# Kernel optimization log

Hardware: AMD Instinct MI355X
Metric: run time of the kernel (lower is better)

## Reference

```python
import jax, jax.numpy as jnp
import numpy as np

B, T, Tc = 64, 256, 16
VW, VC, L = 100000, 128, 25
CE, CH = 25, 25          # char embed / char lstm hidden per direction
WE, WH = 100, 100        # word embed / word lstm hidden per direction (bi -> 200)
DW = WE + 2 * CH         # 150, word-LSTM input dim


def lstm(x, Wih, Whh, b):
    """Unidirectional LSTM over time axis 1. x: [N, S, D] -> [N, S, H]. PyTorch gate order i,f,g,o."""
    N = x.shape[0]
    H = Whh.shape[0]
    x_t = jnp.swapaxes(x, 0, 1)  # [S, N, D]

    def step(carry, xt):
        h, c = carry
        g = xt @ Wih + h @ Whh + b
        i, f, gg, o = jnp.split(g, 4, axis=-1)
        c = jax.nn.sigmoid(f) * c + jax.nn.sigmoid(i) * jnp.tanh(gg)
        h = jax.nn.sigmoid(o) * jnp.tanh(c)
        return (h, c), h

    h0 = jnp.zeros((N, H), x.dtype)
    _, hs = jax.lax.scan(step, (h0, h0), x_t)
    return jnp.swapaxes(hs, 0, 1)  # [N, S, H]


def crf_nll(em, tags, trans, start, end):
    """Negative log-likelihood of linear-chain CRF (no mask; full-length sequences)."""
    # gold path score
    em_score = jnp.take_along_axis(em, tags[:, :, None], axis=2).squeeze(-1).sum(axis=1)
    tr_score = trans[tags[:, :-1], tags[:, 1:]].sum(axis=1)
    gold = start[tags[:, 0]] + em_score + tr_score + end[tags[:, -1]]
    # forward algorithm (log partition)
    alpha0 = start[None, :] + em[:, 0]  # [B, L]

    def step(alpha, e_t):
        # alpha: [B, L] prev-tag scores; trans: [L, L]; e_t: [B, L]
        new = jax.nn.logsumexp(alpha[:, :, None] + trans[None, :, :] + e_t[:, None, :], axis=1)
        return new, None

    alpha, _ = jax.lax.scan(step, alpha0, jnp.swapaxes(em[:, 1:], 0, 1))
    logZ = jax.nn.logsumexp(alpha + end[None, :], axis=1)
    return jnp.sum(logZ - gold)


def setup_inputs():
    key = jax.random.key(0)
    ks = jax.random.split(key, 24)
    f = lambda i, shape: jax.random.normal(ks[i], shape, jnp.float32) * 0.1
    return {
        "tok_tensor": jax.random.randint(ks[0], (B, T), 0, VW),
        "tag_tensor": jax.random.randint(ks[1], (B, T), 0, L),
        "lengths": jnp.full((B,), T, jnp.int32),
        "char_tensor": jax.random.randint(ks[2], (B * T, Tc), 0, VC),
        "char_lengths": jax.random.randint(ks[3], (B * T,), 1, Tc + 1),
        "char_tensor_recover": jax.random.permutation(ks[4], B * T),
        "word_emb": f(5, (VW, WE)),
        "char_emb": f(6, (VC, CE)),
        "cWih_f": f(7, (CE, 4 * CH)), "cWhh_f": f(8, (CH, 4 * CH)), "cb_f": jnp.zeros((4 * CH,), jnp.float32),
        "cWih_b": f(9, (CE, 4 * CH)), "cWhh_b": f(10, (CH, 4 * CH)), "cb_b": jnp.zeros((4 * CH,), jnp.float32),
        "wWih_f": f(11, (DW, 4 * WH)), "wWhh_f": f(12, (WH, 4 * WH)), "wb_f": jnp.zeros((4 * WH,), jnp.float32),
        "wWih_b": f(13, (DW, 4 * WH)), "wWhh_b": f(14, (WH, 4 * WH)), "wb_b": jnp.zeros((4 * WH,), jnp.float32),
        "W_tag": f(15, (2 * WH, L)), "b_tag": jnp.zeros((L,), jnp.float32),
        "trans": f(16, (L, L)), "start": f(17, (L,)), "end": f(18, (L,)),
    }


def reference(tok_tensor, tag_tensor, lengths, char_tensor, char_lengths, char_tensor_recover,
              word_emb, char_emb,
              cWih_f, cWhh_f, cb_f, cWih_b, cWhh_b, cb_b,
              wWih_f, wWhh_f, wb_f, wWih_b, wWhh_b, wb_b,
              W_tag, b_tag, trans, start, end):
    N = char_tensor.shape[0]  # B*T words
    # ---- char BiLSTM: last hidden of each direction per word ----
    ce = char_emb[char_tensor]                      # [N, Tc, CE]
    last = char_lengths - 1
    hf = lstm(ce, cWih_f, cWhh_f, cb_f)             # [N, Tc, CH]
    h_fwd = hf[jnp.arange(N), last]                 # forward last valid hidden
    # backward: reverse each word within its length, scan, take hidden at step len-1
    t_ar = jnp.arange(Tc)[None, :]
    rev_idx = jnp.where(t_ar < char_lengths[:, None], char_lengths[:, None] - 1 - t_ar, t_ar)
    ce_rev = jnp.take_along_axis(ce, rev_idx[:, :, None], axis=1)
    hb = lstm(ce_rev, cWih_b, cWhh_b, cb_b)
    h_bwd = hb[jnp.arange(N), last]
    char_feat = jnp.concatenate([h_fwd, h_bwd], axis=-1)[char_tensor_recover].reshape(B, T, 2 * CH)
    # ---- concat word + char features (dropout = identity in eval) ----
    x = jnp.concatenate([word_emb[tok_tensor], char_feat], axis=-1)  # [B, T, DW]
    # ---- word BiLSTM (full-length sequences) ----
    h_f = lstm(x, wWih_f, wWhh_f, wb_f)
    h_b = jnp.flip(lstm(jnp.flip(x, axis=1), wWih_b, wWhh_b, wb_b), axis=1)
    seq = jnp.concatenate([h_f, h_b], axis=-1)       # [B, T, 2*WH]
    # ---- emissions + CRF NLL ----
    em = seq @ W_tag + b_tag                         # [B, T, L]
    return crf_nll(em, tag_tensor, trans, start, end)
```

## Files before the change

kernel.cpp:

```cpp
#include <hip/hip_runtime.h>
#include <hip/hip_bf16.h>

#define NB 64
#define NT 256
#define TC 16
#define NL 25
#define NWORDS 16384
#define DWd 150
#define WEd 100
#define WPB 5

__device__ __forceinline__ float sigf(float x){ return __fdividef(1.f, 1.f + __expf(-x)); }
__device__ __forceinline__ float tanhf_(float x){
    float ax = fabsf(x);
    float e = __expf(-2.f*ax);
    float r = (1.f - e) * __fdividef(1.f, 1.f + e);
    return copysignf(r, x);
}
__device__ __forceinline__ float RL(float v, int k){
    return __int_as_float(__builtin_amdgcn_readlane(__float_as_int(v), k));
}

__global__ void k_zero(int* __restrict__ meta){
  if (threadIdx.x < 34) meta[threadIdx.x] = 0;
}
__global__ __launch_bounds__(256) void k_hist(const int* __restrict__ char_lengths,
                                              int* __restrict__ hist){
  __shared__ int lh[16];
  int tid = threadIdx.x;
  if (tid < 16) lh[tid] = 0;
  __syncthreads();
  int w = blockIdx.x*256 + tid;
  atomicAdd(&lh[char_lengths[w]-1], 1);
  __syncthreads();
  if (tid < 16) atomicAdd(&hist[tid], lh[tid]);
}
__global__ void k_scan(const int* __restrict__ hist, int* __restrict__ cursor){
  if (threadIdx.x == 0){
    int acc = 0;
    for (int i=0;i<16;i++){ cursor[i] = acc; acc += hist[i]; }
  }
}
__global__ __launch_bounds__(256) void k_scatter(const int* __restrict__ char_lengths,
                                                 int* __restrict__ cursor,
                                                 int* __restrict__ widx){
  __shared__ int lh[16], lbase[16];
  int tid = threadIdx.x;
  if (tid < 16) lh[tid] = 0;
  __syncthreads();
  int w = blockIdx.x*256 + tid;
  int len = char_lengths[w]-1;
  int lrank = atomicAdd(&lh[len], 1);
  __syncthreads();
  if (tid < 16) lbase[tid] = atomicAdd(&cursor[tid], lh[tid]);
  __syncthreads();
  widx[lbase[len] + lrank] = w;
}

__global__ void k_gxc(const float* __restrict__ char_emb,
                      const float* __restrict__ cWih_f, const float* __restrict__ cb_f,
                      const float* __restrict__ cWih_b, const float* __restrict__ cb_b,
                      float* __restrict__ gxc){
  int i = blockIdx.x*blockDim.x + threadIdx.x;
  if (i >= 128*2*100) return;
  int col = i % 100; int d = (i/100) & 1; int c = i/200;
  const float* Wih = d ? cWih_b : cWih_f;
  const float* bb  = d ? cb_b  : cb_f;
  float acc = bb[col];
  #pragma unroll
  for (int k=0;k<25;k++) acc += char_emb[c*25+k]*Wih[k*100+col];
  gxc[i] = acc;
}

__global__ __launch_bounds__(512) void k_char(const int* __restrict__ char_tensor,
   const int* __restrict__ char_lengths, const int* __restrict__ widx,
   const float* __restrict__ cWhh_f, const float* __restrict__ cWhh_b,
   const float* __restrict__ gxc, float* __restrict__ cf){
  __shared__ float h_lds[WPB][28];
  __shared__ float act[WPB][100];
  __shared__ int   chars[WPB][TC];
  __shared__ int   lens[WPB];
  __shared__ int   wids[WPB];
  int tid = threadIdx.x;
  int d  = blockIdx.x & 1;
  int wb = blockIdx.x >> 1;
  int w0 = wb*WPB;
  if (tid < WPB){
    int slot = w0 + tid; if (slot > NWORDS-1) slot = NWORDS-1;
    wids[tid] = widx[slot];
  }
  __syncthreads();
  if (tid < WPB*TC){
    int ww = wids[tid/TC];
    chars[tid/TC][tid%TC] = char_tensor[ww*TC + (tid%TC)];
  }
  if (tid < WPB) lens[tid] = char_lengths[wids[tid]];
  int wsub = tid/100;
  int j    = tid - wsub*100;
  bool gate_thr = tid < WPB*100;
  const float* Wh = d ? cWhh_b : cWhh_f;
  float wcol[25];
  if (gate_thr){
    #pragma unroll
    for (int k=0;k<25;k++) wcol[k] = Wh[k*100 + j];
  }
  if (gate_thr && j < 28) h_lds[wsub][j] = 0.f;
  float c_reg = 0.f, h_last = 0.f;
  __syncthreads();
  int lmax = lens[0];
  #pragma unroll
  for (int q=1;q<WPB;q++) lmax = max(lmax, lens[q]);
  int len = gate_thr ? lens[wsub] : 1;
  bool isg = (j >= 50) && (j < 75);
  float gnext = 0.f;
  if (gate_thr){
    int ci = d ? (len-1) : 0;
    if (ci < 0 || ci >= TC) ci = 0;
    gnext = gxc[(size_t)(chars[wsub][ci]*2+d)*100 + j];
  }
  for (int t=0;t<lmax;t++){
    float gcur = gnext;
    if (gate_thr && t+1 < TC){
      int ci = d ? (len-2-t) : (t+1);
      if (ci < 0 || ci >= TC) ci = 0;
      gnext = gxc[(size_t)(chars[wsub][ci]*2+d)*100 + j];
    }
    if (gate_thr){
      float a0 = gcur, a1 = 0.f, a2 = 0.f, a3 = 0.f;
      const float4* h4 = (const float4*)h_lds[wsub];
      #pragma unroll
      for (int kq=0;kq<6;kq++){
        float4 hq = h4[kq];
        a0 += hq.x*wcol[4*kq];
        a1 += hq.y*wcol[4*kq+1];
        a2 += hq.z*wcol[4*kq+2];
        a3 += hq.w*wcol[4*kq+3];
      }
      a0 += h_lds[wsub][24]*wcol[24];
      float a = (a0+a1)+(a2+a3);
      act[wsub][j] = isg ? tanhf_(a) : sigf(a);
    }
    __syncthreads();
    if (gate_thr && j < 25 && t < len){
      float si = act[wsub][j], sf = act[wsub][25+j], sg = act[wsub][50+j], so = act[wsub][75+j];
      c_reg = sf*c_reg + si*sg;
      float hv = so*tanhf_(c_reg);
      h_lds[wsub][j] = hv;
      h_last = hv;
    }
    __syncthreads();
  }
  if (gate_thr && j < 25){
    int w = wids[wsub];
    cf[(size_t)w*56 + d*28 + j] = h_last;
  }
}

__global__ __launch_bounds__(256) void k_wih(const int* __restrict__ tok,
    const int* __restrict__ recover,
    const float* __restrict__ word_emb, const float* __restrict__ cf,
    const float* __restrict__ Wf, const float* __restrict__ bf,
    const float* __restrict__ Wb, const float* __restrict__ bbias,
    float* __restrict__ gx){
  __shared__ float As[150][72];
  __shared__ int toks[64], recs[64];
  int tid = threadIdx.x;
  int m0 = (blockIdx.x>>2)*64;
  int nt = blockIdx.x & 3;
  int n0 = nt*256;
  if (tid < 64) toks[tid] = tok[m0 + tid];
  else if (tid < 128) recs[tid-64] = recover[m0 + tid - 64];
  __syncthreads();
  for (int i=tid; i<64*150; i+=256){
    int r = i/150; int k = i - r*150;
    float v;
    if (k < WEd) v = word_emb[(long)toks[r]*WEd + k];
    else {
      int ci = k - WEd;
      int dd = ci/25; int uu = ci - dd*25;
      v = cf[(size_t)recs[r]*56 + dd*28 + uu];
    }
    As[k][r] = v;
  }
  __syncthreads();
  int tn = tid & 31; int tm = tid >> 5;
  int j0 = n0 + tn*8;
  bool colok = j0 < 800;
  int d = (j0 >= 400) ? 1 : 0;
  const float* W = d ? Wb : Wf;
  int jc = j0 - d*400;
  float acc[8][8];
  #pragma unroll
  for (int mi=0;mi<8;mi++)
    #pragma unroll
    for (int ni=0;ni<8;ni++) acc[mi][ni]=0.f;
  if (colok){
    for (int k=0;k<150;k++){
      float4 b0 = *(const float4*)&W[k*400 + jc];
      float4 b1 = *(const float4*)&W[k*400 + jc + 4];
      float4 a0 = *(const float4*)&As[k][tm*8];
      float4 a1 = *(const float4*)&As[k][tm*8+4];
      float av[8] = {a0.x,a0.y,a0.z,a0.w,a1.x,a1.y,a1.z,a1.w};
      float bv[8] = {b0.x,b0.y,b0.z,b0.w,b1.x,b1.y,b1.z,b1.w};
      #pragma unroll
      for (int mi=0;mi<8;mi++)
        #pragma unroll
        for (int ni=0;ni<8;ni++) acc[mi][ni] += av[mi]*bv[ni];
    }
    const float* bptr = d ? bbias : bf;
    float bias[8];
    #pragma unroll
    for (int ni=0;ni<8;ni++) bias[ni] = bptr[jc+ni];
    #pragma unroll
    for (int mi=0;mi<8;mi++){
      int p = m0 + tm*8 + mi;
      float* orow = gx + ((long)d*NWORDS + p)*400 + jc;
      #pragma unroll
      for (int ni=0;ni<8;ni++) orow[ni] = acc[mi][ni] + bias[ni];
    }
  }
}

__global__ __launch_bounds__(448, 2) void k_wlstm(const float* __restrict__ gx,
     const float* __restrict__ Whf, const float* __restrict__ Whb,
     float* __restrict__ hseq){
  __shared__ float wstage[10000];
  __shared__ float h_lds[100];
  __shared__ float act[400];
  int tid = threadIdx.x;
  int s = blockIdx.x & 63; int d = blockIdx.x >> 6;
  const float* Wh = d ? Whb : Whf;
  int j = tid;
  bool colthr = j < 400;
  float wreg[100];
  #pragma unroll
  for (int ch=0; ch<4; ch++){
    for (int i=tid; i<2500; i+=448)
      ((float4*)wstage)[i] = ((const float4*)(Wh + ch*10000))[i];
    __syncthreads();
    if (colthr){
      #pragma unroll
      for (int kk=0;kk<25;kk++) wreg[ch*25+kk] = wstage[kk*400 + j];
    }
    __syncthreads();
  }
  if (tid < 100) h_lds[tid] = 0.f;
  float c_reg = 0.f;
  const float* gxd = gx + ((long)d*NWORDS + (long)s*256)*400;
  bool isg = (j >= 200) && (j < 300);
  __syncthreads();
  float gnext = 0.f;
  if (colthr) gnext = gxd[(d?255:0)*400 + j];
  for (int t=0;t<256;t++){
    float gcur = gnext;
    if (colthr && t+1 < 256){
      int tn = d ? (255-(t+1)) : (t+1);
      gnext = gxd[tn*400 + j];
    }
    if (colthr){
      float a0 = gcur, a1 = 0.f, a2 = 0.f, a3 = 0.f;
      const float4* h4 = (const float4*)h_lds;
      #pragma unroll
      for (int kq=0;kq<25;kq++){
        float4 hq = h4[kq];
        a0 += hq.x*wreg[4*kq];
        a1 += hq.y*wreg[4*kq+1];
        a2 += hq.z*wreg[4*kq+2];
        a3 += hq.w*wreg[4*kq+3];
      }
      float a = (a0+a1)+(a2+a3);
      act[j] = isg ? tanhf_(a) : sigf(a);
    }
    __syncthreads();
    if (tid < 100){
      float si = act[tid], sf = act[100+tid], sg = act[200+tid], so = act[300+tid];
      c_reg = sf*c_reg + si*sg;
      float hv = so*tanhf_(c_reg);
      h_lds[tid] = hv;
      int ttc = d ? (255-t) : t;
      hseq[((long)d*NWORDS + s*256 + ttc)*100 + tid] = hv;
    }
    __syncthreads();
  }
}

__global__ __launch_bounds__(256) void k_em(const float* __restrict__ hseq,
    const float* __restrict__ Wtag, const float* __restrict__ btag,
    float* __restrict__ em){
  __shared__ float hrow[8][200];
  __shared__ float Ws[5000];
  int tid = threadIdx.x;
  for (int i=tid;i<5000;i+=256) Ws[i] = Wtag[i];
  int p0 = blockIdx.x*8;
  for (int i=tid;i<8*200;i+=256){
    int r = i/200; int k = i - r*200;
    int p = p0+r;
    hrow[r][k] = (k<100) ? hseq[(long)p*100+k] : hseq[((long)NWORDS + p)*100 + (k-100)];
  }
  __syncthreads();
  int r = tid>>5; int c = tid&31;
  if (c<25){
    float acc = btag[c];
    for (int k=0;k<200;k++) acc += hrow[r][k]*Ws[k*25+c];
    em[(long)(p0+r)*25 + c] = acc;
  }
}

__global__ __launch_bounds__(64) void k_crf(const float* __restrict__ em,
    const int* __restrict__ tag, const float* __restrict__ trans,
    const float* __restrict__ start, const float* __restrict__ endv,
    float* __restrict__ part){
  int s = blockIdx.x;
  int lane = threadIdx.x;
  const float* emb = em + (long)s*256*25;
  float tr[25];
  #pragma unroll
  for (int k=0;k<25;k++) tr[k] = (lane<25) ? trans[k*25+lane] : 0.f;
  float alpha = (lane<25) ? (start[lane] + emb[lane]) : 0.f;
  float enext = (lane<25) ? emb[25+lane] : 0.f;
  for (int t=1;t<256;t++){
    float ecur = enext;
    if (t<255 && lane<25) enext = emb[(t+1)*25 + lane];
    float base = RL(alpha, 0);
    float s0=0.f,s1=0.f,s2=0.f,s3=0.f,s4=0.f;
    #pragma unroll
    for (int k=0;k<5;k++) s0 += __expf(RL(alpha,k)    + tr[k]    - base);
    #pragma unroll
    for (int k=0;k<5;k++) s1 += __expf(RL(alpha,5+k)  + tr[5+k]  - base);
    #pragma unroll
    for (int k=0;k<5;k++) s2 += __expf(RL(alpha,10+k) + tr[10+k] - base);
    #pragma unroll
    for (int k=0;k<5;k++) s3 += __expf(RL(alpha,15+k) + tr[15+k] - base);
    #pragma unroll
    for (int k=0;k<5;k++) s4 += __expf(RL(alpha,20+k) + tr[20+k] - base);
    float ssum = ((s0+s1)+(s2+s3))+s4;
    alpha = __logf(ssum) + base + ecur;
  }
  float val = (lane<25) ? (alpha + endv[lane]) : -1e30f;
  float m2 = -1e30f;
  #pragma unroll
  for (int k=0;k<25;k++) m2 = fmaxf(m2, RL(val,k));
  float s2s = 0.f;
  #pragma unroll
  for (int k=0;k<25;k++) s2s += __expf(RL(val,k) - m2);
  float logZ = __logf(s2s) + m2;
  const int* tg = tag + s*256;
  float gp = 0.f;
  for (int t=lane; t<256; t+=64){
    int a = tg[t];
    gp += emb[t*25 + a];
    if (t<255) gp += trans[a*25 + tg[t+1]];
  }
  #pragma unroll
  for (int off=32; off; off>>=1) gp += __shfl_xor(gp, off, 64);
  if (lane==0){
    float gold = gp + start[tg[0]] + endv[tg[255]];
    part[s] = logZ - gold;
  }
}

__global__ __launch_bounds__(64) void k_red(const float* __restrict__ part, float* __restrict__ out){
  float v = part[threadIdx.x];
  #pragma unroll
  for (int off=32; off; off>>=1) v += __shfl_xor(v, off, 64);
  if (threadIdx.x==0) out[0] = v;
}

extern "C" void kernel_launch(void* const* d_in, const int* in_sizes, int n_in,
                              void* d_out, int out_size, void* d_ws, size_t ws_size,
                              hipStream_t stream){
  const int* tok          = (const int*)d_in[0];
  const int* tagp         = (const int*)d_in[1];
  const int* char_tensor  = (const int*)d_in[3];
  const int* char_lengths = (const int*)d_in[4];
  const int* recover      = (const int*)d_in[5];
  const float* word_emb = (const float*)d_in[6];
  const float* char_emb = (const float*)d_in[7];
  const float* cWih_f=(const float*)d_in[8];  const float* cWhh_f=(const float*)d_in[9];  const float* cb_f=(const float*)d_in[10];
  const float* cWih_b=(const float*)d_in[11]; const float* cWhh_b=(const float*)d_in[12]; const float* cb_b=(const float*)d_in[13];
  const float* wWih_f=(const float*)d_in[14]; const float* wWhh_f=(const float*)d_in[15]; const float* wb_f=(const float*)d_in[16];
  const float* wWih_b=(const float*)d_in[17]; const float* wWhh_b=(const float*)d_in[18]; const float* wb_b=(const float*)d_in[19];
  const float* W_tag=(const float*)d_in[20];  const float* b_tag=(const float*)d_in[21];
  const float* trans=(const float*)d_in[22];  const float* startv=(const float*)d_in[23]; const float* endv=(const float*)d_in[24];

  float* ws  = (float*)d_ws;
  float* gxc = ws;
  float* cf  = ws + 25600;
  float* gx  = ws + 943104;
  float* hseq= ws + 14050304;
  float* em  = ws;
  float* part= ws + 17327104;
  int*   meta= (int*)(ws + 17327168);
  int*   widx= meta + 64;
  float* out = (float*)d_out;

  k_zero   <<<1,   64,  0, stream>>>(meta);
  k_gxc    <<<100, 256, 0, stream>>>(char_emb, cWih_f, cb_f, cWih_b, cb_b, gxc);
  k_hist   <<<64,  256, 0, stream>>>(char_lengths, meta);
  k_scan   <<<1,   64,  0, stream>>>(meta, meta+16);
  k_scatter<<<64,  256, 0, stream>>>(char_lengths, meta+16, widx);
  k_char   <<<6554,512, 0, stream>>>(char_tensor, char_lengths, widx, cWhh_f, cWhh_b, gxc, cf);
  k_wih    <<<1024,256, 0, stream>>>(tok, recover, word_emb, cf, wWih_f, wb_f, wWih_b, wb_b, gx);
  k_wlstm  <<<128, 448, 0, stream>>>(gx, wWhh_f, wWhh_b, hseq);
  k_em     <<<2048,256, 0, stream>>>(hseq, W_tag, b_tag, em);
  k_crf    <<<64,  64,  0, stream>>>(em, tagp, trans, startv, endv, part);
  k_red    <<<1,   64,  0, stream>>>(part, out);
}
```

Before: 536.2 us.

## Shuffle-based char LSTM gates, transposed emission weights, exp-domain CRF recursion

The char LSTM kernel now interleaves the four gates of each hidden unit across adjacent lanes and combines them with cross-lane shuffles. It double-buffers the hidden state in LDS, which removes one of the two block barriers per timestep and the activation staging buffer. The emission kernel stores the tag weights transposed and padded so it can use float4 LDS reads. The CRF forward pass precomputes exp(trans) and does the inner sum as multiplies instead of 25 exps per lane per step, which can lose numerical range because the only stabiliser is lane 0's alpha.

```diff
diff --git a/kernel.cpp b/kernel.cpp
--- a/kernel.cpp
+++ b/kernel.cpp
@@ -76,8 +76,7 @@
    const int* __restrict__ char_lengths, const int* __restrict__ widx,
    const float* __restrict__ cWhh_f, const float* __restrict__ cWhh_b,
    const float* __restrict__ gxc, float* __restrict__ cf){
-  __shared__ float h_lds[WPB][28];
-  __shared__ float act[WPB][100];
+  __shared__ float h_lds[2][WPB][28];
   __shared__ int   chars[WPB][TC];
   __shared__ int   lens[WPB];
   __shared__ int   wids[WPB];
@@ -95,39 +94,46 @@
     chars[tid/TC][tid%TC] = char_tensor[ww*TC + (tid%TC)];
   }
   if (tid < WPB) lens[tid] = char_lengths[wids[tid]];
+  if (tid < 2*WPB*28){
+    int p = tid/(WPB*28); int rr = tid - p*WPB*28;
+    h_lds[p][rr/28][rr%28] = 0.f;
+  }
   int wsub = tid/100;
-  int j    = tid - wsub*100;
+  int r    = tid - wsub*100;
+  int u    = r >> 2;
+  int gid  = r & 3;
   bool gate_thr = tid < WPB*100;
+  int col = gid*25 + u;
   const float* Wh = d ? cWhh_b : cWhh_f;
   float wcol[25];
   if (gate_thr){
     #pragma unroll
-    for (int k=0;k<25;k++) wcol[k] = Wh[k*100 + j];
-  }
-  if (gate_thr && j < 28) h_lds[wsub][j] = 0.f;
+    for (int k=0;k<25;k++) wcol[k] = Wh[k*100 + col];
+  }
   float c_reg = 0.f, h_last = 0.f;
   __syncthreads();
   int lmax = lens[0];
   #pragma unroll
   for (int q=1;q<WPB;q++) lmax = max(lmax, lens[q]);
   int len = gate_thr ? lens[wsub] : 1;
-  bool isg = (j >= 50) && (j < 75);
+  bool isg = (gid == 2);
   float gnext = 0.f;
   if (gate_thr){
     int ci = d ? (len-1) : 0;
     if (ci < 0 || ci >= TC) ci = 0;
-    gnext = gxc[(size_t)(chars[wsub][ci]*2+d)*100 + j];
+    gnext = gxc[(size_t)(chars[wsub][ci]*2+d)*100 + col];
   }
   for (int t=0;t<lmax;t++){
     float gcur = gnext;
     if (gate_thr && t+1 < TC){
       int ci = d ? (len-2-t) : (t+1);
       if (ci < 0 || ci >= TC) ci = 0;
-      gnext = gxc[(size_t)(chars[wsub][ci]*2+d)*100 + j];
-    }
+      gnext = gxc[(size_t)(chars[wsub][ci]*2+d)*100 + col];
+    }
+    float x = 0.f;
     if (gate_thr){
       float a0 = gcur, a1 = 0.f, a2 = 0.f, a3 = 0.f;
-      const float4* h4 = (const float4*)h_lds[wsub];
+      const float4* h4 = (const float4*)h_lds[t&1][wsub];
       #pragma unroll
       for (int kq=0;kq<6;kq++){
         float4 hq = h4[kq];
@@ -136,23 +142,27 @@
         a2 += hq.z*wcol[4*kq+2];
         a3 += hq.w*wcol[4*kq+3];
       }
-      a0 += h_lds[wsub][24]*wcol[24];
+      a0 += h_lds[t&1][wsub][24]*wcol[24];
       float a = (a0+a1)+(a2+a3);
-      act[wsub][j] = isg ? tanhf_(a) : sigf(a);
+      x = isg ? tanhf_(a) : sigf(a);
+    }
+    float A = __shfl_xor(x, 1, 64);
+    float B = __shfl_xor(x, 2, 64);
+    float C = __shfl_xor(B, 1, 64);
+    if (gate_thr && gid == 0){
+      float hv;
+      if (t < len){
+        c_reg = A*c_reg + x*B;
+        hv = C*tanhf_(c_reg);
+        h_last = hv;
+      } else hv = h_last;
+      h_lds[(t+1)&1][wsub][u] = hv;
     }
     __syncthreads();
-    if (gate_thr && j < 25 && t < len){
-      float si = act[wsub][j], sf = act[wsub][25+j], sg = act[wsub][50+j], so = act[wsub][75+j];
-      c_reg = sf*c_reg + si*sg;
-      float hv = so*tanhf_(c_reg);
-      h_lds[wsub][j] = hv;
-      h_last = hv;
-    }
-    __syncthreads();
-  }
-  if (gate_thr && j < 25){
+  }
+  if (gate_thr && gid == 0){
     int w = wids[wsub];
-    cf[(size_t)w*56 + d*28 + j] = h_last;
+    cf[(size_t)w*56 + d*28 + u] = h_last;
   }
 }
 
@@ -288,9 +298,12 @@
     const float* __restrict__ Wtag, const float* __restrict__ btag,
     float* __restrict__ em){
   __shared__ float hrow[8][200];
-  __shared__ float Ws[5000];
-  int tid = threadIdx.x;
-  for (int i=tid;i<5000;i+=256) Ws[i] = Wtag[i];
+  __shared__ float WsT[25][204];
+  int tid = threadIdx.x;
+  for (int i=tid;i<5000;i+=256){
+    int c = i/200; int k = i - c*200;
+    WsT[c][k] = Wtag[k*25 + c];
+  }
   int p0 = blockIdx.x*8;
   for (int i=tid;i<8*200;i+=256){
     int r = i/200; int k = i - r*200;
@@ -300,9 +313,15 @@
   __syncthreads();
   int r = tid>>5; int c = tid&31;
   if (c<25){
-    float acc = btag[c];
-    for (int k=0;k<200;k++) acc += hrow[r][k]*Ws[k*25+c];
-    em[(long)(p0+r)*25 + c] = acc;
+    float a0=0.f,a1=0.f,a2=0.f,a3=0.f;
+    #pragma unroll 10
+    for (int k=0;k<200;k+=4){
+      float4 h4 = *(const float4*)&hrow[r][k];
+      float4 w4 = *(const float4*)&WsT[c][k];
+      a0 += h4.x*w4.x; a1 += h4.y*w4.y;
+      a2 += h4.z*w4.z; a3 += h4.w*w4.w;
+    }
+    em[(long)(p0+r)*25 + c] = btag[c] + (a0+a1)+(a2+a3);
   }
 }
 
@@ -313,26 +332,27 @@
   int s = blockIdx.x;
   int lane = threadIdx.x;
   const float* emb = em + (long)s*256*25;
-  float tr[25];
-  #pragma unroll
-  for (int k=0;k<25;k++) tr[k] = (lane<25) ? trans[k*25+lane] : 0.f;
+  float etr[25];
+  #pragma unroll
+  for (int k=0;k<25;k++) etr[k] = (lane<25) ? __expf(trans[k*25+lane]) : 0.f;
   float alpha = (lane<25) ? (start[lane] + emb[lane]) : 0.f;
   float enext = (lane<25) ? emb[25+lane] : 0.f;
   for (int t=1;t<256;t++){
     float ecur = enext;
     if (t<255 && lane<25) enext = emb[(t+1)*25 + lane];
     float base = RL(alpha, 0);
+    float e = __expf(alpha - base);
     float s0=0.f,s1=0.f,s2=0.f,s3=0.f,s4=0.f;
     #pragma unroll
-    for (int k=0;k<5;k++) s0 += __expf(RL(alpha,k)    + tr[k]    - base);
-    #pragma unroll
-    for (int k=0;k<5;k++) s1 += __expf(RL(alpha,5+k)  + tr[5+k]  - base);
-    #pragma unroll
-    for (int k=0;k<5;k++) s2 += __expf(RL(alpha,10+k) + tr[10+k] - base);
-    #pragma unroll
-    for (int k=0;k<5;k++) s3 += __expf(RL(alpha,15+k) + tr[15+k] - base);
-    #pragma unroll
-    for (int k=0;k<5;k++) s4 += __expf(RL(alpha,20+k) + tr[20+k] - base);
+    for (int k=0;k<5;k++) s0 += RL(e,k)    * etr[k];
+    #pragma unroll
+    for (int k=0;k<5;k++) s1 += RL(e,5+k)  * etr[5+k];
+    #pragma unroll
+    for (int k=0;k<5;k++) s2 += RL(e,10+k) * etr[10+k];
+    #pragma unroll
+    for (int k=0;k<5;k++) s3 += RL(e,15+k) * etr[15+k];
+    #pragma unroll
+    for (int k=0;k<5;k++) s4 += RL(e,20+k) * etr[20+k];
     float ssum = ((s0+s1)+(s2+s3))+s4;
     alpha = __logf(ssum) + base + ecur;
   }
```

Measured after the change: 521.7 us. -2.7%, faster.
